# Optimization experiments

Measured on AMD Instinct MI355X. Metric: run time of the kernel, lower is better.

The kernel has to match this reference:

```python
import jax, jax.numpy as jnp
import numpy as np

B, TM1, N, H = 2048, 128, 64, 128  # batch, T-1, input_size (num series), hidden


def setup_inputs() -> dict:
    key = jax.random.key(0)
    ks = jax.random.split(key, 9)
    s = 0.05  # small init scale for weights
    return {
        "X": jax.random.normal(ks[0], (B, TM1, N), jnp.float32),
        "W_attn1": jax.random.normal(ks[1], (TM1, 2 * H + TM1), jnp.float32) * s,
        "b_attn1": jax.random.normal(ks[2], (TM1,), jnp.float32) * s,
        "w_attn2": jax.random.normal(ks[3], (TM1,), jnp.float32) * s,
        "b_attn2": jax.random.normal(ks[4], (1,), jnp.float32) * s,
        "W_ih": jax.random.normal(ks[5], (4 * H, N), jnp.float32) * s,
        "W_hh": jax.random.normal(ks[6], (4 * H, H), jnp.float32) * s,
        "b_ih": jax.random.normal(ks[7], (4 * H,), jnp.float32) * s,
        "b_hh": jax.random.normal(ks[8], (4 * H,), jnp.float32) * s,
    }


def reference(X, W_attn1, b_attn1, w_attn2, b_attn2, W_ih, W_hh, b_ih, b_hh):
    Bb, Tm1, Nn = X.shape
    Hh = W_hh.shape[1]
    # attention first-layer weight split: [h | s | series] columns
    W1_h = W_attn1[:, :Hh]          # (Tm1, H)
    W1_s = W_attn1[:, Hh:2 * Hh]    # (Tm1, H)
    W1_x = W_attn1[:, 2 * Hh:]      # (Tm1, Tm1)
    Xp = jnp.swapaxes(X, 1, 2)      # (B, N, Tm1) full series per driver
    # series contribution to attention is constant over time -> precompute
    pre_x = jnp.einsum('bnt,kt->bnk', Xp, W1_x) + b_attn1  # (B, N, Tm1)
    b_lstm = b_ih + b_hh

    def step(carry, x_t):
        h, c = carry  # each (B, H); c is the LSTM cell state (s_n in torch code)
        z = jnp.tanh(pre_x + (h @ W1_h.T)[:, None, :] + (c @ W1_s.T)[:, None, :])  # (B,N,Tm1)
        e = z @ w_attn2 + b_attn2              # (B, N)
        alpha = jax.nn.softmax(e, axis=1)      # softmax over input drivers
        x_tilde = alpha * x_t                  # (B, N)
        gates = x_tilde @ W_ih.T + h @ W_hh.T + b_lstm  # (B, 4H)
        i, f, g, o = jnp.split(gates, 4, axis=1)        # torch gate order i,f,g,o
        c_new = jax.nn.sigmoid(f) * c + jax.nn.sigmoid(i) * jnp.tanh(g)
        h_new = jax.nn.sigmoid(o) * jnp.tanh(c_new)
        return (h_new, c_new), h_new

    h0 = jnp.zeros((Bb, Hh), X.dtype)
    (_, _), hs = jax.lax.scan(step, (h0, h0), jnp.swapaxes(X, 0, 1))  # hs: (Tm1, B, H)
    return jnp.swapaxes(hs, 0, 1)  # (B, Tm1, H) == X_encoded
```

## Files before the change

### kernel.cpp

```cpp
#include <hip/hip_runtime.h>
#include <hip/hip_fp16.h>


typedef float f32x4 __attribute__((ext_vector_type(4)));
typedef _Float16 f16x8 __attribute__((ext_vector_type(8)));
typedef _Float16 f16x4 __attribute__((ext_vector_type(4)));

#define LOG2E 1.44269504088896340736f
__device__ __forceinline__ float rcpf(float x){ return __builtin_amdgcn_rcpf(x); }
__device__ __forceinline__ float fast_exp(float x){ return __builtin_exp2f(x * LOG2E); }
__device__ __forceinline__ float fast_tanh(float x){
  float e = __builtin_exp2f(x * (2.0f * LOG2E));
  return 1.0f - 2.0f * rcpf(e + 1.0f);
}
__device__ __forceinline__ float fast_sig(float x){
  float e = __builtin_exp2f(x * (-LOG2E));
  return rcpf(1.0f + e);
}
__device__ __forceinline__ float sx(float v, int m){ return __shfl_xor(v, m, 64); }

__global__ __launch_bounds__(256) void k0_wt(const float* __restrict__ Wat, float* __restrict__ Wt){
  int idx = blockIdx.x*256 + threadIdx.x;
  int t = idx >> 7, k = idx & 127;
  Wt[idx] = Wat[k*384 + 256 + t];
}
__global__ __launch_bounds__(256) void k0_p1p(const float* __restrict__ Wat, _Float16* __restrict__ p1p){
  int idx = blockIdx.x*256 + threadIdx.x;
  int e = idx & 7, l = (idx>>3) & 63, f = (idx>>9) & 7, w = idx >> 12;
  int col = w*16 + (l & 15);
  int c   = f*32 + ((l>>4)&3)*8 + e;
  p1p[idx] = (_Float16)Wat[col*384 + c];
}
__global__ __launch_bounds__(256) void k0_p4p(const float* __restrict__ Wih, const float* __restrict__ Whh,
                                              _Float16* __restrict__ p4p){
  int idx = blockIdx.x*256 + threadIdx.x;
  int e = idx & 7, l = (idx>>3) & 63, r = idx >> 9;
  int fi = r % 24, w = r / 24;
  int ti = fi / 6, ks = fi % 6;
  int g = (w*4 + ti)*16 + (l & 15);
  int c = ks*32 + ((l>>4)&3)*8 + e;
  p4p[idx] = (_Float16)((c < 64) ? Wih[g*64 + c] : Whh[g*128 + (c-64)]);
}

__global__ __launch_bounds__(256) void k1_prex(const float* __restrict__ X,
                                               const float* __restrict__ Wt,
                                               const float* __restrict__ b1,
                                               __half* __restrict__ prex){
  __shared__ float Xs[128][64];
  const int tid = threadIdx.x;
  const long b = blockIdx.x;
  {
    const float4* X4 = (const float4*)(X + b*8192);
    float4* Xs4 = (float4*)&Xs[0][0];
    #pragma unroll
    for (int i=0;i<8;i++) Xs4[tid + i*256] = X4[tid + i*256];
  }
  __syncthreads();
  const int nq = tid >> 4, kq = tid & 15;
  float acc[4][8];
  #pragma unroll
  for (int n=0;n<4;n++)
    #pragma unroll
    for (int k=0;k<8;k++) acc[n][k]=0.f;
  #pragma unroll 4
  for (int t=0;t<128;t++){
    float4 w0 = *(const float4*)(Wt + t*128 + kq*8);
    float4 w1 = *(const float4*)(Wt + t*128 + kq*8 + 4);
    float4 xv = *(const float4*)&Xs[t][nq*4];
    float wv[8] = {w0.x,w0.y,w0.z,w0.w,w1.x,w1.y,w1.z,w1.w};
    float xa[4] = {xv.x,xv.y,xv.z,xv.w};
    #pragma unroll
    for (int n=0;n<4;n++)
      #pragma unroll
      for (int k=0;k<8;k++) acc[n][k] = fmaf(xa[n], wv[k], acc[n][k]);
  }
  float4 bv0 = *(const float4*)(b1 + kq*8);
  float4 bv1 = *(const float4*)(b1 + kq*8 + 4);
  #pragma unroll
  for (int n=0;n<4;n++){
    __half* dst = prex + ((long)(b*64 + nq*4 + n))*128 + kq*8;
    union { __half2 h2[4]; uint4 u4; } pk;
    pk.h2[0] = __floats2half2_rn(acc[n][0]+bv0.x, acc[n][1]+bv0.y);
    pk.h2[1] = __floats2half2_rn(acc[n][2]+bv0.z, acc[n][3]+bv0.w);
    pk.h2[2] = __floats2half2_rn(acc[n][4]+bv1.x, acc[n][5]+bv1.y);
    pk.h2[3] = __floats2half2_rn(acc[n][6]+bv1.z, acc[n][7]+bv1.w);
    *(uint4*)dst = pk.u4;
  }
}

__global__ __launch_bounds__(512, 2)
void k2_lstm(const float* __restrict__ X,
             const _Float16* __restrict__ p1p,
             const _Float16* __restrict__ p4p,
             const float* __restrict__ w2,
             const float* __restrict__ bih,
             const float* __restrict__ bhh,
             const __half* __restrict__ prex,
             float* __restrict__ out)
{
  const int tid = threadIdx.x;
  const long b0 = (long)blockIdx.x * 4;
  const int w = tid >> 6, l = tid & 63;

  __shared__ alignas(16) _Float16 A1[16*264];
  __shared__ alignas(16) _Float16 A4[16*200];
  __shared__ float aa[4][128];
  __shared__ float gp[4][512];
  __shared__ float epp[256][2];

  for (int i = tid; i < 16*264; i += 512) A1[i] = (_Float16)0.f;
  for (int i = tid; i < 16*200; i += 512) A4[i] = (_Float16)0.f;

  f16x8 w1f[8];
  {
    const f16x8* p = (const f16x8*)p1p;
    #pragma unroll
    for (int f = 0; f < 8; ++f) w1f[f] = p[(w*8 + f)*64 + l];
  }
  f16x8 w4f[24];
  {
    const f16x8* p = (const f16x8*)p4p;
    #pragma unroll
    for (int f = 0; f < 24; ++f) w4f[f] = p[(w*24 + f)*64 + l];
  }

  const int kq = tid & 31, p2ns = (tid >> 5) & 3, p2b = tid >> 7;
  f16x4 pxr[16];
  {
    const _Float16* pb = (const _Float16*)prex + ((b0 + p2b)*64 + p2ns*16)*128 + kq*4;
    #pragma unroll
    for (int i = 0; i < 16; ++i) pxr[i] = *(const f16x4*)(pb + i*128);
  }
  const f32x4 w2v = *(const f32x4*)(w2 + kq*4);

  const int arow = l & 15, ag = l >> 4;

  const int ob = tid >> 7, oj = tid & 127;
  const float bl0 = bih[oj]       + bhh[oj];
  const float bl1 = bih[oj + 128] + bhh[oj + 128];
  const float bl2 = bih[oj + 256] + bhh[oj + 256];
  const float bl3 = bih[oj + 384] + bhh[oj + 384];
  float cre = 0.f;

  __syncthreads();

  for (int t = 0; t < 128; ++t) {
    {
      f32x4 acc = {0.f,0.f,0.f,0.f};
      const _Float16* Ab = A1 + arow*264 + ag*8;
      #pragma unroll
      for (int f = 0; f < 8; ++f) {
        f16x8 a = *(const f16x8*)(Ab + f*32);
        acc = __builtin_amdgcn_mfma_f32_16x16x32_f16(a, w1f[f], acc, 0, 0, 0);
      }
      if (l < 16) {
        #pragma unroll
        for (int v = 0; v < 4; ++v) aa[v][w*16 + l] = acc[v];
      }
    }
    __syncthreads();

    {
      f32x4 aq = *(const f32x4*)&aa[p2b][kq*4];
      #pragma unroll
      for (int i = 0; i < 16; ++i) {
        f16x4 p = pxr[i];
        float e = fmaf(fast_tanh((float)p[0] + aq.x), w2v.x,
                  fmaf(fast_tanh((float)p[1] + aq.y), w2v.y,
                  fmaf(fast_tanh((float)p[2] + aq.z), w2v.z,
                       fast_tanh((float)p[3] + aq.w) * w2v.w)));
        e += sx(e, 1);
        e += sx(e, 2);
        e += sx(e, 4);
        e += sx(e, 8);
        if ((kq & 15) == 0) epp[p2b*64 + p2ns*16 + i][kq >> 4] = e;
      }
    }
    __syncthreads();

    if (tid < 256) {
      int b = tid >> 6, n = tid & 63;
      float e = epp[tid][0] + epp[tid][1];
      float mx = e;
      #pragma unroll
      for (int m = 32; m >= 1; m >>= 1) mx = fmaxf(mx, sx(mx, m));
      float p = fast_exp(e - mx);
      float sm = p;
      #pragma unroll
      for (int m = 32; m >= 1; m >>= 1) sm += sx(sm, m);
      float xtv = p * rcpf(sm) * X[(b0+b)*8192 + (long)t*64 + n];
      A4[b*200 + n] = (_Float16)xtv;
    }
    __syncthreads();

    {
      f32x4 c0 = {0.f,0.f,0.f,0.f}, c1 = c0, c2 = c0, c3 = c0;
      const _Float16* Ab = A4 + arow*200 + ag*8;
      #pragma unroll
      for (int ks = 0; ks < 6; ++ks) {
        f16x8 a = *(const f16x8*)(Ab + ks*32);
        c0 = __builtin_amdgcn_mfma_f32_16x16x32_f16(a, w4f[ks],      c0, 0, 0, 0);
        c1 = __builtin_amdgcn_mfma_f32_16x16x32_f16(a, w4f[6  + ks], c1, 0, 0, 0);
        c2 = __builtin_amdgcn_mfma_f32_16x16x32_f16(a, w4f[12 + ks], c2, 0, 0, 0);
        c3 = __builtin_amdgcn_mfma_f32_16x16x32_f16(a, w4f[18 + ks], c3, 0, 0, 0);
      }
      if (l < 16) {
        #pragma unroll
        for (int v = 0; v < 4; ++v) {
          gp[v][(w*4 + 0)*16 + l] = c0[v];
          gp[v][(w*4 + 1)*16 + l] = c1[v];
          gp[v][(w*4 + 2)*16 + l] = c2[v];
          gp[v][(w*4 + 3)*16 + l] = c3[v];
        }
      }
    }
    __syncthreads();

    {
      float s0 = gp[ob][oj]       + bl0;
      float s1 = gp[ob][oj + 128] + bl1;
      float s2 = gp[ob][oj + 256] + bl2;
      float s3 = gp[ob][oj + 384] + bl3;
      float ig = fast_sig(s0), fg = fast_sig(s1);
      float gg = fast_tanh(s2), og = fast_sig(s3);
      cre = fmaf(fg, cre, ig*gg);
      float hn = og * fast_tanh(cre);
      _Float16 hh = (_Float16)hn;
      A1[ob*264 + oj]       = hh;
      A1[ob*264 + 128 + oj] = (_Float16)cre;
      A4[ob*200 + 64 + oj]  = hh;
      out[(b0+ob)*16384 + (long)t*128 + oj] = hn;
    }
    __syncthreads();
  }
}

extern "C" void kernel_launch(void* const* d_in, const int* in_sizes, int n_in,
                              void* d_out, int out_size, void* d_ws, size_t ws_size,
                              hipStream_t stream) {
  const float* X   = (const float*)d_in[0];
  const float* Wat = (const float*)d_in[1];
  const float* b1  = (const float*)d_in[2];
  const float* w2  = (const float*)d_in[3];
  const float* Wih = (const float*)d_in[5];
  const float* Whh = (const float*)d_in[6];
  const float* bih = (const float*)d_in[7];
  const float* bhh = (const float*)d_in[8];
  float* out  = (float*)d_out;

  float*    Wt   = (float*)d_ws;
  _Float16* p1p  = (_Float16*)(Wt + 16384);
  _Float16* p4p  = (_Float16*)(Wt + 32768);
  __half*   prexH= (__half*)(Wt + 81920);

  k0_wt  <<<64,  256, 0, stream>>>(Wat, Wt);
  k0_p1p <<<128, 256, 0, stream>>>(Wat, p1p);
  k0_p4p <<<384, 256, 0, stream>>>(Wih, Whh, p4p);
  k1_prex<<<2048,256, 0, stream>>>(X, Wt, b1, prexH);
  k2_lstm<<<512, 512, 0, stream>>>(X, p1p, p4p, w2, bih, bhh, prexH, out);
}
```

Measured before the change: 1.633 ms.

## Process eight batch rows per LSTM block to fill MFMA rows and halve blocks

Each workgroup of the recurrent kernel now handles 8 batch rows instead of 4, so more of the 16-row MFMA tiles carry useful data. The grid shrinks from 512 to 256 blocks. Work is remapped so each wave owns one batch row for the attention tanh and the softmax, with the X value prefetched into a register at the top of each step. Each thread updates two LSTM cells. This amortises the per-timestep barriers and MFMA issue over twice the batch, at the cost of more registers (32 prex vectors per thread), possible lower occupancy, and fewer blocks to spread across the compute units.

```diff
diff --git a/kernel.cpp b/kernel.cpp
--- a/kernel.cpp
+++ b/kernel.cpp
@@ -99,14 +99,14 @@
              float* __restrict__ out)
 {
   const int tid = threadIdx.x;
-  const long b0 = (long)blockIdx.x * 4;
+  const long b0 = (long)blockIdx.x * 8;
   const int w = tid >> 6, l = tid & 63;
 
   __shared__ alignas(16) _Float16 A1[16*264];
   __shared__ alignas(16) _Float16 A4[16*200];
-  __shared__ float aa[4][128];
-  __shared__ float gp[4][512];
-  __shared__ float epp[256][2];
+  __shared__ float aa[8][128];
+  __shared__ float gp[8][512];
+  __shared__ float epp[8][64][2];
 
   for (int i = tid; i < 16*264; i += 512) A1[i] = (_Float16)0.f;
   for (int i = tid; i < 16*200; i += 512) A4[i] = (_Float16)0.f;
@@ -124,12 +124,12 @@
     for (int f = 0; f < 24; ++f) w4f[f] = p[(w*24 + f)*64 + l];
   }
 
-  const int kq = tid & 31, p2ns = (tid >> 5) & 3, p2b = tid >> 7;
-  f16x4 pxr[16];
-  {
-    const _Float16* pb = (const _Float16*)prex + ((b0 + p2b)*64 + p2ns*16)*128 + kq*4;
-    #pragma unroll
-    for (int i = 0; i < 16; ++i) pxr[i] = *(const f16x4*)(pb + i*128);
+  const int kq = l & 31, ng = l >> 5;
+  f16x4 pxr[32];
+  {
+    const _Float16* pb = (const _Float16*)prex + ((b0 + w)*64 + ng*32)*128 + kq*4;
+    #pragma unroll
+    for (int i = 0; i < 32; ++i) pxr[i] = *(const f16x4*)(pb + i*128);
   }
   const f32x4 w2v = *(const f32x4*)(w2 + kq*4);
 
@@ -140,11 +140,15 @@
   const float bl1 = bih[oj + 128] + bhh[oj + 128];
   const float bl2 = bih[oj + 256] + bhh[oj + 256];
   const float bl3 = bih[oj + 384] + bhh[oj + 384];
-  float cre = 0.f;
+  float cre0 = 0.f, cre1 = 0.f;
+
+  float xreg = 0.f;
 
   __syncthreads();
 
   for (int t = 0; t < 128; ++t) {
+    xreg = X[(b0 + w)*8192 + (long)t*64 + l];
+
     {
       f32x4 acc = {0.f,0.f,0.f,0.f};
       const _Float16* Ab = A1 + arow*264 + ag*8;
@@ -153,17 +157,18 @@
         f16x8 a = *(const f16x8*)(Ab + f*32);
         acc = __builtin_amdgcn_mfma_f32_16x16x32_f16(a, w1f[f], acc, 0, 0, 0);
       }
-      if (l < 16) {
+      if (l < 32) {
+        int rb = (l >> 4) * 4;
         #pragma unroll
-        for (int v = 0; v < 4; ++v) aa[v][w*16 + l] = acc[v];
-      }
-    }
-    __syncthreads();
-
-    {
-      f32x4 aq = *(const f32x4*)&aa[p2b][kq*4];
-      #pragma unroll
-      for (int i = 0; i < 16; ++i) {
+        for (int v = 0; v < 4; ++v) aa[rb + v][w*16 + (l & 15)] = acc[v];
+      }
+    }
+    __syncthreads();
+
+    {
+      f32x4 aq = *(const f32x4*)&aa[w][kq*4];
+      #pragma unroll
+      for (int i = 0; i < 32; ++i) {
         f16x4 p = pxr[i];
         float e = fmaf(fast_tanh((float)p[0] + aq.x), w2v.x,
                   fmaf(fast_tanh((float)p[1] + aq.y), w2v.y,
@@ -173,14 +178,13 @@
         e += sx(e, 2);
         e += sx(e, 4);
         e += sx(e, 8);
-        if ((kq & 15) == 0) epp[p2b*64 + p2ns*16 + i][kq >> 4] = e;
-      }
-    }
-    __syncthreads();
-
-    if (tid < 256) {
-      int b = tid >> 6, n = tid & 63;
-      float e = epp[tid][0] + epp[tid][1];
+        if ((kq & 15) == 0) epp[w][ng*32 + i][kq >> 4] = e;
+      }
+    }
+    __syncthreads();
+
+    {
+      float e = epp[w][l][0] + epp[w][l][1];
       float mx = e;
       #pragma unroll
       for (int m = 32; m >= 1; m >>= 1) mx = fmaxf(mx, sx(mx, m));
@@ -188,8 +192,8 @@
       float sm = p;
       #pragma unroll
       for (int m = 32; m >= 1; m >>= 1) sm += sx(sm, m);
-      float xtv = p * rcpf(sm) * X[(b0+b)*8192 + (long)t*64 + n];
-      A4[b*200 + n] = (_Float16)xtv;
+      float xtv = p * rcpf(sm) * xreg;
+      A4[w*200 + l] = (_Float16)xtv;
     }
     __syncthreads();
 
@@ -204,13 +208,14 @@
         c2 = __builtin_amdgcn_mfma_f32_16x16x32_f16(a, w4f[12 + ks], c2, 0, 0, 0);
         c3 = __builtin_amdgcn_mfma_f32_16x16x32_f16(a, w4f[18 + ks], c3, 0, 0, 0);
       }
-      if (l < 16) {
+      if (l < 32) {
+        int rb = (l >> 4) * 4, col = l & 15;
         #pragma unroll
         for (int v = 0; v < 4; ++v) {
-          gp[v][(w*4 + 0)*16 + l] = c0[v];
-          gp[v][(w*4 + 1)*16 + l] = c1[v];
-          gp[v][(w*4 + 2)*16 + l] = c2[v];
-          gp[v][(w*4 + 3)*16 + l] = c3[v];
+          gp[rb + v][(w*4 + 0)*16 + col] = c0[v];
+          gp[rb + v][(w*4 + 1)*16 + col] = c1[v];
+          gp[rb + v][(w*4 + 2)*16 + col] = c2[v];
+          gp[rb + v][(w*4 + 3)*16 + col] = c3[v];
         }
       }
     }
@@ -223,13 +228,26 @@
       float s3 = gp[ob][oj + 384] + bl3;
       float ig = fast_sig(s0), fg = fast_sig(s1);
       float gg = fast_tanh(s2), og = fast_sig(s3);
-      cre = fmaf(fg, cre, ig*gg);
-      float hn = og * fast_tanh(cre);
-      _Float16 hh = (_Float16)hn;
-      A1[ob*264 + oj]       = hh;
-      A1[ob*264 + 128 + oj] = (_Float16)cre;
-      A4[ob*200 + 64 + oj]  = hh;
-      out[(b0+ob)*16384 + (long)t*128 + oj] = hn;
+      cre0 = fmaf(fg, cre0, ig*gg);
+      float hn0 = og * fast_tanh(cre0);
+      float u0 = gp[ob+4][oj]       + bl0;
+      float u1 = gp[ob+4][oj + 128] + bl1;
+      float u2 = gp[ob+4][oj + 256] + bl2;
+      float u3 = gp[ob+4][oj + 384] + bl3;
+      float ih = fast_sig(u0), fh = fast_sig(u1);
+      float gh = fast_tanh(u2), oh = fast_sig(u3);
+      cre1 = fmaf(fh, cre1, ih*gh);
+      float hn1 = oh * fast_tanh(cre1);
+
+      _Float16 h0 = (_Float16)hn0, h1 = (_Float16)hn1;
+      A1[ob*264 + oj]           = h0;
+      A1[ob*264 + 128 + oj]     = (_Float16)cre0;
+      A4[ob*200 + 64 + oj]      = h0;
+      A1[(ob+4)*264 + oj]       = h1;
+      A1[(ob+4)*264 + 128 + oj] = (_Float16)cre1;
+      A4[(ob+4)*200 + 64 + oj]  = h1;
+      out[(b0+ob)*16384   + (long)t*128 + oj] = hn0;
+      out[(b0+ob+4)*16384 + (long)t*128 + oj] = hn1;
     }
     __syncthreads();
   }
@@ -257,5 +275,5 @@
   k0_p1p <<<128, 256, 0, stream>>>(Wat, p1p);
   k0_p4p <<<384, 256, 0, stream>>>(Wih, Whh, p4p);
   k1_prex<<<2048,256, 0, stream>>>(X, Wt, b1, prexH);
-  k2_lstm<<<512, 512, 0, stream>>>(X, p1p, p4p, w2, bih, bhh, prexH, out);
-}
+  k2_lstm<<<256, 512, 0, stream>>>(X, p1p, p4p, w2, bih, bhh, prexH, out);
+}
```

After: 2.105 ms. +28.9%, slower.
